# Kernel optimization log

Measured on AMD Instinct MI355X. Metric: run time of the kernel, lower is better.

## Reference

```python
import jax, jax.numpy as jnp
import numpy as np

NUM_HEADS = 12
AGENT_NUM = 49

def setup_inputs() -> dict:
    key = jax.random.key(0)
    ks = jax.random.split(key, 5)
    B, N, C = 32, 1176, 768
    x = jax.random.normal(ks[0], (B, N, C), dtype=jnp.float32)
    qkv_w = jax.random.normal(ks[1], (3 * C, C), dtype=jnp.float32) * 0.02
    qkv_b = jax.random.normal(ks[2], (3 * C,), dtype=jnp.float32) * 0.02
    proj_w = jax.random.normal(ks[3], (C, C), dtype=jnp.float32) * 0.02
    proj_b = jax.random.normal(ks[4], (C,), dtype=jnp.float32) * 0.02
    return {"x": x, "qkv_w": qkv_w, "qkv_b": qkv_b, "proj_w": proj_w,
            "proj_b": proj_b, "t_h": 14, "t_w": 14, "s_h": 28, "s_w": 28}

def _softmax_clamped(a):
    # original: float32 clamp to finfo min/max, then softmax(dim=-1)
    fi = jnp.finfo(jnp.float32)
    a = jnp.clip(a.astype(jnp.float32), fi.min, fi.max)
    return jax.nn.softmax(a, axis=-1)

def reference(x, qkv_w, qkv_b, proj_w, proj_b, t_h, t_w, s_h, s_w):
    B, N, C = x.shape
    H = NUM_HEADS
    hd = C // H
    scale = hd ** -0.5
    n_mt = 2 * t_h * t_w
    n_s = s_h * s_w

    qkv = (x @ qkv_w.T + qkv_b).reshape(B, N, 3, H, hd).transpose(2, 0, 3, 1, 4)
    q, k, v = qkv[0], qkv[1], qkv[2]  # [B,H,N,hd]

    q_mt, q_s = q[:, :, :n_mt], q[:, :, n_mt:]
    k_mt = k[:, :, :n_mt]
    v_mt = v[:, :, :n_mt]

    # stage 1: template/memory self-attention
    attn = _softmax_clamped(jnp.einsum('bhqd,bhkd->bhqk', q_mt, k_mt) * scale)
    x_mt = jnp.einsum('bhqk,bhkd->bhqd', attn, v_mt).transpose(0, 2, 1, 3).reshape(B, n_mt, C)

    # agent tokens: pool q_s (replicates original layout-scrambling reshape)
    p = int(AGENT_NUM ** 0.5)  # 7
    agent = q_s.reshape(B, s_h, s_w, C).transpose(0, 3, 1, 2)  # [B,C,s_h,s_w]
    agent = agent.reshape(B, C, p, s_h // p, p, s_w // p).mean(axis=(3, 5))  # exact AdaptiveAvgPool2d(7,7)
    agent = agent.reshape(B, C, AGENT_NUM).transpose(0, 2, 1)  # [B,agent_num,C]
    agent = agent.reshape(B, AGENT_NUM, H, hd).transpose(0, 2, 1, 3)  # [B,H,agent_num,hd]

    # stage 2: agent attends to all keys
    agent_attn = _softmax_clamped(jnp.einsum('bhad,bhkd->bhak', agent * scale, k))
    agent_v = jnp.einsum('bhak,bhkd->bhad', agent_attn, v)  # [B,H,agent_num,hd]

    # stage 3: search queries attend to agent tokens
    q_attn = _softmax_clamped(jnp.einsum('bhqd,bhad->bhqa', q_s * scale, agent))
    x_s = jnp.einsum('bhqa,bhad->bhqd', q_attn, agent_v).transpose(0, 2, 1, 3).reshape(B, n_s, C)

    out = jnp.concatenate([x_mt, x_s], axis=1)
    out = out @ proj_w.T + proj_b
    return out
```

## Files before the change

kernel.cpp:

```cpp
#include <hip/hip_runtime.h>

typedef __attribute__((ext_vector_type(8))) short short8;
typedef __attribute__((ext_vector_type(4))) short short4v;
typedef __attribute__((ext_vector_type(4))) float f32x4;
typedef unsigned short u16;

#define B_    32
#define N_    1176
#define C_    768
#define H_    12
#define HD_   64
#define NMT_  392
#define AG_   49
#define NEGBIG_ (-1.0e4f)

__device__ __forceinline__ u16 f2bf(float f) {
  unsigned u = __float_as_uint(f);
  unsigned r = (u + 0x7fffu + ((u >> 16) & 1u)) >> 16;
  return (u16)r;
}
__device__ __forceinline__ float bf2f(u16 s) {
  return __uint_as_float(((unsigned)s) << 16);
}

__device__ __forceinline__ int xcd_swz(int g, int nwg) {
  const int q = nwg >> 3, r = nwg & 7;
  const int xcd = g & 7, off = g >> 3;
  return (xcd < r ? xcd * (q + 1) : r * (q + 1) + (xcd - r) * q) + off;
}

template <int LO>
__global__ __launch_bounds__(256) void splitf(const float* __restrict__ in,
                                              u16* __restrict__ hi,
                                              u16* __restrict__ lo, int n4) {
  int i = blockIdx.x * 256 + threadIdx.x;
  const int stride = gridDim.x * 256;
  for (; i < n4; i += stride) {
    const float4 v = ((const float4*)in)[i];
    const float f[4] = {v.x, v.y, v.z, v.w};
    short4v h, l;
#pragma unroll
    for (int e = 0; e < 4; ++e) {
      u16 hb = f2bf(f[e]);
      h[e] = (short)hb;
      if (LO) l[e] = (short)f2bf(f[e] - bf2f(hb));
    }
    ((short4v*)hi)[i] = h;
    if (LO) ((short4v*)lo)[i] = l;
  }
}

__global__ __launch_bounds__(256, 3) void gemm_qkv(
    const u16* __restrict__ A, const u16* __restrict__ Bw,
    const float* __restrict__ bias, u16* __restrict__ qb, u16* __restrict__ kb,
    u16* __restrict__ vb, int Mch) {
  __shared__ u16 SH[17408];
  u16* As = SH;
  u16* Bs = SH + 8192;
  const int tid = threadIdx.x;
  const int swz = xcd_swz(blockIdx.x, gridDim.x);
  const int brow = swz / 18, bcol = swz - brow * 18;
  const int m0 = brow * 128, c0 = bcol * 128;
  const int lane = tid & 63, w = tid >> 6;
  const int wr = w >> 1, wc = w & 1;
  const int fr = lane & 15, ko = lane >> 4;
  const int lsw = (lane * 8) ^ (ko << 4);

  f32x4 acc[4][4];
#pragma unroll
  for (int m = 0; m < 4; ++m)
#pragma unroll
    for (int n = 0; n < 4; ++n) acc[m][n] = (f32x4)0.f;

  short8 ra[4], rb[4];
  auto LOADG = [&](int kt) {
#pragma unroll
    for (int i = 0; i < 4; ++i) {
      const int ch = tid + i * 256;
      const int row = ch >> 3, slotk = ch & 7;
      const int ar = min(m0 + row, Mch - 1);
      ra[i] = *(const short8*)&A[(size_t)ar * 768 + kt * 64 + slotk * 8];
      rb[i] = *(const short8*)&Bw[(size_t)(c0 + row) * 768 + kt * 64 + slotk * 8];
    }
  };
  auto WRITE = [&]() {
#pragma unroll
    for (int i = 0; i < 4; ++i) {
      const int ch = tid + i * 256;
      const int row = ch >> 3, slotk = ch & 7;
      const int s = slotk >> 2, sl = slotk & 3;
      const int off = (row >> 4) * 1024 + s * 512 +
                      ((sl * 128 + (row & 15) * 8) ^ (sl << 4));
      *(short8*)&As[off] = ra[i];
      *(short8*)&Bs[off] = rb[i];
    }
  };

  LOADG(0);
  for (int kt = 0; kt < 12; ++kt) {
    __syncthreads();
    WRITE();
    if (kt < 11) LOADG(kt + 1);
    __syncthreads();
#pragma unroll
    for (int s = 0; s < 2; ++s) {
      short8 af[4], bfr[4];
#pragma unroll
      for (int m = 0; m < 4; ++m)
        af[m] = *(const short8*)&As[((wr * 4 + m) * 2 + s) * 512 + lsw];
#pragma unroll
      for (int n = 0; n < 4; ++n)
        bfr[n] = *(const short8*)&Bs[((wc * 4 + n) * 2 + s) * 512 + lsw];
#pragma unroll
      for (int m = 0; m < 4; ++m)
#pragma unroll
        for (int n = 0; n < 4; ++n)
          acc[m][n] = __builtin_amdgcn_mfma_f32_16x16x32_bf16(af[m], bfr[n], acc[m][n], 0, 0, 0);
    }
  }

  __syncthreads();
  const int t = c0 / 768;
  const int hbase = (c0 % 768) >> 6;
  if (t < 2) {
#pragma unroll
    for (int n = 0; n < 4; ++n) {
      const int col = wc * 64 + n * 16 + fr;
      const float bv = bias[c0 + col];
#pragma unroll
      for (int m = 0; m < 4; ++m)
#pragma unroll
        for (int r = 0; r < 4; ++r) {
          const int row = wr * 64 + m * 16 + ko * 4 + r;
          SH[row * 136 + col] = f2bf(acc[m][n][r] + bv);
        }
    }
    __syncthreads();
    u16* dst = (t == 0) ? qb : kb;
    for (int it = tid; it < 2048; it += 256) {
      const int rt = it >> 4, half = (it >> 3) & 1, p = it & 7;
      const int mg = m0 + rt;
      if (mg < Mch) {
        const int bl = mg / N_, nt = mg - bl * N_;
        const short8 vv = *(const short8*)&SH[rt * 136 + half * 64 + p * 8];
        *(short8*)&dst[(((size_t)bl * H_ + hbase + half) * N_ + nt) * 64 + p * 8] = vv;
      }
    }
  } else {
#pragma unroll
    for (int n = 0; n < 4; ++n) {
      const int col = wc * 64 + n * 16 + fr;
      const float bv = bias[c0 + col];
#pragma unroll
      for (int m = 0; m < 4; ++m)
#pragma unroll
        for (int r = 0; r < 4; ++r) {
          const int row = wr * 64 + m * 16 + ko * 4 + r;
          SH[col * 136 + row] = f2bf(acc[m][n][r] + bv);
        }
    }
    __syncthreads();
    for (int it = tid; it < 2048; it += 256) {
      const int ct = it >> 4, tc = it & 15;
      const int mg0 = m0 + tc * 8;
      if (mg0 < Mch) {
        const int bl = mg0 / N_, nt = mg0 - bl * N_;
        const int d = ct & 63, hh = hbase + (ct >> 6);
        const short8 vv = *(const short8*)&SH[ct * 136 + tc * 8];
        *(short8*)&vb[(((size_t)bl * H_ + hh) * 64 + d) * N_ + nt] = vv;
      }
    }
  }
}

__global__ __launch_bounds__(256, 2) void gemm_proj(
    const u16* __restrict__ Ahg, const u16* __restrict__ Alg,
    const u16* __restrict__ Bhg, const u16* __restrict__ Blg,
    const float* __restrict__ bias, float* __restrict__ out) {
  __shared__ u16 Ah[8192], Al[8192], Bh[8192], Bl[8192];
  const int tid = threadIdx.x;
  const int swz = xcd_swz(blockIdx.x, gridDim.x);
  const int brow = swz / 6, bcol = swz - brow * 6;
  const int m0 = brow * 128, c0 = bcol * 128;
  const int lane = tid & 63, w = tid >> 6;
  const int wr = w >> 1, wc = w & 1;
  const int fr = lane & 15, ko = lane >> 4;
  const int lsw = (lane * 8) ^ (ko << 4);

  f32x4 acc[4][4];
#pragma unroll
  for (int m = 0; m < 4; ++m)
#pragma unroll
    for (int n = 0; n < 4; ++n) acc[m][n] = (f32x4)0.f;

  short8 rah[4], ral[4], rbh[4], rbl[4];
  auto LOADG = [&](int kt) {
#pragma unroll
    for (int i = 0; i < 4; ++i) {
      const int ch = tid + i * 256;
      const int row = ch >> 3, slotk = ch & 7;
      const size_t aoff = (size_t)(m0 + row) * 768 + kt * 64 + slotk * 8;
      const size_t boff = (size_t)(c0 + row) * 768 + kt * 64 + slotk * 8;
      rah[i] = *(const short8*)&Ahg[aoff];
      ral[i] = *(const short8*)&Alg[aoff];
      rbh[i] = *(const short8*)&Bhg[boff];
      rbl[i] = *(const short8*)&Blg[boff];
    }
  };
  auto WRITE = [&]() {
#pragma unroll
    for (int i = 0; i < 4; ++i) {
      const int ch = tid + i * 256;
      const int row = ch >> 3, slotk = ch & 7;
      const int s = slotk >> 2, sl = slotk & 3;
      const int off = (row >> 4) * 1024 + s * 512 +
                      ((sl * 128 + (row & 15) * 8) ^ (sl << 4));
      *(short8*)&Ah[off] = rah[i];
      *(short8*)&Al[off] = ral[i];
      *(short8*)&Bh[off] = rbh[i];
      *(short8*)&Bl[off] = rbl[i];
    }
  };

  LOADG(0);
  for (int kt = 0; kt < 12; ++kt) {
    __syncthreads();
    WRITE();
    if (kt < 11) LOADG(kt + 1);
    __syncthreads();
#pragma unroll
    for (int s = 0; s < 2; ++s) {
      short8 ah[4], al[4], bh[4], bl[4];
#pragma unroll
      for (int m = 0; m < 4; ++m) {
        const int off = ((wr * 4 + m) * 2 + s) * 512 + lsw;
        ah[m] = *(const short8*)&Ah[off];
        al[m] = *(const short8*)&Al[off];
      }
#pragma unroll
      for (int n = 0; n < 4; ++n) {
        const int off = ((wc * 4 + n) * 2 + s) * 512 + lsw;
        bh[n] = *(const short8*)&Bh[off];
        bl[n] = *(const short8*)&Bl[off];
      }
#pragma unroll
      for (int m = 0; m < 4; ++m)
#pragma unroll
        for (int n = 0; n < 4; ++n) {
          acc[m][n] = __builtin_amdgcn_mfma_f32_16x16x32_bf16(ah[m], bh[n], acc[m][n], 0, 0, 0);
          acc[m][n] = __builtin_amdgcn_mfma_f32_16x16x32_bf16(ah[m], bl[n], acc[m][n], 0, 0, 0);
          acc[m][n] = __builtin_amdgcn_mfma_f32_16x16x32_bf16(al[m], bh[n], acc[m][n], 0, 0, 0);
        }
    }
  }
#pragma unroll
  for (int n = 0; n < 4; ++n) {
    const int col = c0 + wc * 64 + n * 16 + fr;
    const float bv = bias[col];
#pragma unroll
    for (int m = 0; m < 4; ++m) {
      const int mg = m0 + wr * 64 + m * 16 + ko * 4;
#pragma unroll
      for (int r = 0; r < 4; ++r) out[(size_t)(mg + r) * 768 + col] = acc[m][n][r] + bv;
    }
  }
}

__global__ __launch_bounds__(256) void agent_pool(const u16* __restrict__ q,
                                                  u16* __restrict__ agent) {
  const int wid = threadIdx.x >> 6;
  const int lane = threadIdx.x & 63;
  const int row = blockIdx.x * 4 + wid;
  const int rem = row % (H_ * 64);
  const int b = row / (H_ * 64);
  const int h2 = rem / 64;
  const int a = rem % 64;
  if (a >= AG_) {
    agent[((size_t)b * H_ + h2) * 4096 + a * 64 + lane] = 0;
    return;
  }
  const int ap = a / 7, aq = a % 7;
  float s = 0.f;
#pragma unroll
  for (int i = 0; i < 4; ++i)
#pragma unroll
    for (int j = 0; j < 4; ++j) {
      const int g = (ap * 4 + i) * 336 + (aq * 4 + j) * 12 + h2;
      const int h = g / 784, n = g % 784;
      s += bf2f(q[(((size_t)b * H_ + h) * N_ + NMT_ + n) * HD_ + lane]);
    }
  agent[((size_t)b * H_ + h2) * 4096 + a * 64 + lane] = f2bf(s * 0.0625f);
}

__global__ __launch_bounds__(256, 3) void flash_attn(
    const u16* __restrict__ Q, int q_bh_str, int q_base, int q_row_max, int q_valid,
    const u16* __restrict__ K, int k_bh_str, int k_row_max,
    const u16* __restrict__ Vt, int vt_bh_str, int vt_pitch, int vt_col_max,
    int n_keys, int nkt,
    u16* __restrict__ cch, u16* __restrict__ ccl, int b0,
    u16* __restrict__ avT, int mode) {
  __shared__ u16 Qs[4096], Ks[4096], Vts[4096], Ps[4096];
  __shared__ float Ss[64][65];
  __shared__ float mS[64], lS[64], aS[64];

  const int tid = threadIdx.x, bh = blockIdx.x;
  const int q0 = q_base + blockIdx.y * 56;
  const int lane = tid & 63, w = tid >> 6;
  const int fr = lane & 15, ko = lane >> 4;

  const u16* Qb = Q + (size_t)bh * q_bh_str;
  const u16* Kb = K + (size_t)bh * k_bh_str;
  const u16* Vb = Vt + (size_t)bh * vt_bh_str;

#pragma unroll
  for (int i = 0; i < 2; ++i) {
    const int ch = tid + i * 256;
    const int row = ch >> 3, c8 = (ch & 7) << 3;
    const int qr = min(q0 + row, q_row_max);
    const short8 v = *(const short8*)&Qb[(size_t)qr * 64 + c8];
    *(short8*)&Qs[(row * 64 + c8) ^ ((row & 7) << 3)] = v;
  }
  if (tid < 64) { mS[tid] = NEGBIG_; lS[tid] = 0.f; aS[tid] = 0.f; }

  f32x4 oacc[4];
#pragma unroll
  for (int d = 0; d < 4; ++d) oacc[d] = (f32x4)0.f;

  for (int kt = 0; kt < nkt; ++kt) {
#pragma unroll
    for (int i = 0; i < 2; ++i) {
      const int ch = tid + i * 256;
      const int row = ch >> 3, c8 = (ch & 7) << 3;
      const int kr = min(kt * 64 + row, k_row_max);
      const short8 v = *(const short8*)&Kb[(size_t)kr * 64 + c8];
      *(short8*)&Ks[(row * 64 + c8) ^ ((row & 7) << 3)] = v;
    }
#pragma unroll
    for (int i = 0; i < 2; ++i) {
      const int ch = tid + i * 256;
      const int row = ch >> 3, c8 = (ch & 7) << 3;
      const int col8 = kt * 64 + c8;
      const u16* src = &Vb[(size_t)row * vt_pitch];
      short8 v;
      if (col8 + 8 <= vt_col_max) {
        v = *(const short8*)&src[col8];
      } else {
#pragma unroll
        for (int e = 0; e < 8; ++e) v[e] = (short)src[min(col8 + e, vt_col_max - 1)];
      }
      *(short8*)&Vts[(row * 64 + c8) ^ ((row & 7) << 3)] = v;
    }
    __syncthreads();

    short8 aq[2];
#pragma unroll
    for (int s = 0; s < 2; ++s)
      aq[s] = *(const short8*)&Qs[((w * 16 + fr) * 64 + s * 32 + ko * 8) ^ ((fr & 7) << 3)];
#pragma unroll
    for (int j = 0; j < 4; ++j) {
      f32x4 sa = (f32x4)0.f;
#pragma unroll
      for (int s = 0; s < 2; ++s) {
        const short8 bk = *(const short8*)&Ks[((j * 16 + fr) * 64 + s * 32 + ko * 8) ^ ((fr & 7) << 3)];
        sa = __builtin_amdgcn_mfma_f32_16x16x32_bf16(aq[s], bk, sa, 0, 0, 0);
      }
      const int colg = kt * 64 + j * 16 + fr;
      const bool maskc = (colg >= n_keys);
#pragma unroll
      for (int r = 0; r < 4; ++r) {
        const int srow = w * 16 + ko * 4 + r;
        Ss[srow][j * 16 + fr] = maskc ? NEGBIG_ : sa[r] * 0.125f;
      }
    }
    __syncthreads();

    {
      const int r = tid >> 2, jj = tid & 3;
      float sv[16];
      float mx = NEGBIG_;
#pragma unroll
      for (int c = 0; c < 16; ++c) {
        sv[c] = Ss[r][jj * 16 + c];
        mx = fmaxf(mx, sv[c]);
      }
      mx = fmaxf(mx, __shfl_xor(mx, 1));
      mx = fmaxf(mx, __shfl_xor(mx, 2));
      const float mold = mS[r];
      const float mnew = fmaxf(mold, mx);
      float sum = 0.f;
#pragma unroll
      for (int c = 0; c < 16; ++c) {
        const bool mk = (kt * 64 + jj * 16 + c) >= n_keys;
        const float p = mk ? 0.f : __expf(sv[c] - mnew);
        sum += p;
        Ps[(r * 64 + jj * 16 + c) ^ ((r & 7) << 3)] = f2bf(p);
      }
      sum += __shfl_xor(sum, 1);
      sum += __shfl_xor(sum, 2);
      if (jj == 0) {
        const float alpha = __expf(mold - mnew);
        aS[r] = alpha;
        lS[r] = lS[r] * alpha + sum;
        mS[r] = mnew;
      }
    }
    __syncthreads();

    float al[4];
#pragma unroll
    for (int r = 0; r < 4; ++r) al[r] = aS[w * 16 + ko * 4 + r];
    short8 ap[2];
#pragma unroll
    for (int s = 0; s < 2; ++s)
      ap[s] = *(const short8*)&Ps[((w * 16 + fr) * 64 + s * 32 + ko * 8) ^ ((fr & 7) << 3)];
#pragma unroll
    for (int dj = 0; dj < 4; ++dj) {
      f32x4 o = oacc[dj];
#pragma unroll
      for (int r = 0; r < 4; ++r) o[r] *= al[r];
#pragma unroll
      for (int s = 0; s < 2; ++s) {
        const short8 bv = *(const short8*)&Vts[((dj * 16 + fr) * 64 + s * 32 + ko * 8) ^ ((fr & 7) << 3)];
        o = __builtin_amdgcn_mfma_f32_16x16x32_bf16(ap[s], bv, o, 0, 0, 0);
      }
      oacc[dj] = o;
    }
    __syncthreads();
  }

  float linv[4];
#pragma unroll
  for (int r = 0; r < 4; ++r) linv[r] = 1.f / fmaxf(lS[w * 16 + ko * 4 + r], 1e-30f);

  if (mode == 0) {
    const int b = bh / H_, h = bh % H_;
#pragma unroll
    for (int dj = 0; dj < 4; ++dj)
#pragma unroll
      for (int r = 0; r < 4; ++r) {
        const int rowl = w * 16 + ko * 4 + r;
        if (rowl < q_valid) {
          const size_t m = (size_t)(b0 + b) * N_ + q0 + rowl;
          const float val = oacc[dj][r] * linv[r];
          const u16 hb = f2bf(val);
          const u16 lb = f2bf(val - bf2f(hb));
          const size_t idx = m * 768 + h * 64 + dj * 16 + fr;
          cch[idx] = hb;
          ccl[idx] = lb;
        }
      }
  } else {
#pragma unroll
    for (int dj = 0; dj < 4; ++dj)
#pragma unroll
      for (int r = 0; r < 4; ++r) {
        const int a = w * 16 + ko * 4 + r;
        avT[(size_t)bh * 4096 + (dj * 16 + fr) * 64 + a] = f2bf(oacc[dj][r] * linv[r]);
      }
  }
}

extern "C" void kernel_launch(void* const* d_in, const int* in_sizes, int n_in,
                              void* d_out, int out_size, void* d_ws,
                              size_t ws_size, hipStream_t stream) {
  const float* x = (const float*)d_in[0];
  const float* qkv_w = (const float*)d_in[1];
  const float* qkv_b = (const float*)d_in[2];
  const float* proj_w = (const float*)d_in[3];
  const float* proj_b = (const float*)d_in[4];
  float* out = (float*)d_out;
  u16* ws = (u16*)d_ws;

  const size_t XBF = 28901376ull;
  const size_t QW = 2304ull * 768;
  const size_t PW = 768ull * 768;
  const size_t QKV1 = (size_t)H_ * N_ * HD_;
  const size_t AG1 = (size_t)H_ * 64 * 64;

  size_t o = 0;
  u16* xbf = ws + o; o += XBF;
  u16* qwh = ws + o; o += QW;
  u16* pwh = ws + o; o += PW;
  u16* pwl = ws + o; o += PW;
  u16* cch = ws + o; o += XBF;
  u16* ccl = ws + o; o += XBF;
  const size_t fixed_sh = o;
  const size_t per_sh = 3 * QKV1 + 2 * AG1;

  int cb = 1;
  const int cands[6] = {32, 16, 8, 4, 2, 1};
  for (int i = 0; i < 6; ++i)
    if ((fixed_sh + (size_t)cands[i] * per_sh) * 2 <= ws_size) { cb = cands[i]; break; }

  u16* qb = ws + o; o += cb * QKV1;
  u16* kb = ws + o; o += cb * QKV1;
  u16* vb = ws + o; o += cb * QKV1;
  u16* agent = ws + o; o += cb * AG1;
  u16* avT = ws + o; o += cb * AG1;

  splitf<0><<<2048, 256, 0, stream>>>(x, xbf, nullptr, (int)(XBF / 4));
  splitf<0><<<1024, 256, 0, stream>>>(qkv_w, qwh, nullptr, (int)(QW / 4));
  splitf<1><<<512, 256, 0, stream>>>(proj_w, pwh, pwl, (int)(PW / 4));

  const int nch = B_ / cb;
  for (int chn = 0; chn < nch; ++chn) {
    const int b0 = chn * cb;
    const int Mch = cb * N_;
    const int nrow = (Mch + 127) / 128;
    gemm_qkv<<<dim3(nrow * 18), 256, 0, stream>>>(
        xbf + (size_t)b0 * N_ * 768, qwh, qkv_b, qb, kb, vb, Mch);
    agent_pool<<<dim3(cb * 192), 256, 0, stream>>>(qb, agent);
    flash_attn<<<dim3(cb * H_, 1), 256, 0, stream>>>(
        agent, 4096, 0, 48, AG_, kb, N_ * HD_, N_ - 1,
        vb, N_ * HD_, N_, N_, N_, 19, nullptr, nullptr, b0, avT, 1);
    flash_attn<<<dim3(cb * H_, 7), 256, 0, stream>>>(
        qb, N_ * HD_, 0, N_ - 1, 56, kb, N_ * HD_, N_ - 1,
        vb, N_ * HD_, N_, N_, NMT_, 7, cch, ccl, b0, nullptr, 0);
    flash_attn<<<dim3(cb * H_, 14), 256, 0, stream>>>(
        qb, N_ * HD_, NMT_, N_ - 1, 56, agent, 4096, 63,
        avT, 4096, 64, 64, AG_, 1, cch, ccl, b0, nullptr, 0);
  }
  gemm_proj<<<dim3(294 * 6), 256, 0, stream>>>(cch, ccl, pwh, pwl, proj_b, out);
}
```

Measured before the change: 537.0 us.

## Drop low-bf16 split of attention output and remap QKV GEMM block order

```diff
diff --git a/kernel.cpp b/kernel.cpp
--- a/kernel.cpp
+++ b/kernel.cpp
@@ -59,7 +59,11 @@
   u16* Bs = SH + 8192;
   const int tid = threadIdx.x;
   const int swz = xcd_swz(blockIdx.x, gridDim.x);
-  const int brow = swz / 18, bcol = swz - brow * 18;
+  const int half = gridDim.x >> 1;
+  const int cg = swz / half;
+  const int rem = swz - cg * half;
+  const int brow = rem / 9;
+  const int bcol = cg * 9 + (rem - brow * 9);
   const int m0 = brow * 128, c0 = bcol * 128;
   const int lane = tid & 63, w = tid >> 6;
   const int wr = w >> 1, wc = w & 1;
@@ -138,12 +142,12 @@
     __syncthreads();
     u16* dst = (t == 0) ? qb : kb;
     for (int it = tid; it < 2048; it += 256) {
-      const int rt = it >> 4, half = (it >> 3) & 1, p = it & 7;
+      const int rt = it >> 4, half2 = (it >> 3) & 1, p = it & 7;
       const int mg = m0 + rt;
       if (mg < Mch) {
         const int bl = mg / N_, nt = mg - bl * N_;
-        const short8 vv = *(const short8*)&SH[rt * 136 + half * 64 + p * 8];
-        *(short8*)&dst[(((size_t)bl * H_ + hbase + half) * N_ + nt) * 64 + p * 8] = vv;
+        const short8 vv = *(const short8*)&SH[rt * 136 + half2 * 64 + p * 8];
+        *(short8*)&dst[(((size_t)bl * H_ + hbase + half2) * N_ + nt) * 64 + p * 8] = vv;
       }
     }
   } else {
@@ -173,11 +177,11 @@
   }
 }
 
-__global__ __launch_bounds__(256, 2) void gemm_proj(
-    const u16* __restrict__ Ahg, const u16* __restrict__ Alg,
-    const u16* __restrict__ Bhg, const u16* __restrict__ Blg,
-    const float* __restrict__ bias, float* __restrict__ out) {
-  __shared__ u16 Ah[8192], Al[8192], Bh[8192], Bl[8192];
+__global__ __launch_bounds__(256, 3) void gemm_proj(
+    const u16* __restrict__ Ahg, const u16* __restrict__ Bhg,
+    const u16* __restrict__ Blg, const float* __restrict__ bias,
+    float* __restrict__ out) {
+  __shared__ u16 Ah[8192], Bh[8192], Bl[8192];
   const int tid = threadIdx.x;
   const int swz = xcd_swz(blockIdx.x, gridDim.x);
   const int brow = swz / 6, bcol = swz - brow * 6;
@@ -193,7 +197,7 @@
 #pragma unroll
     for (int n = 0; n < 4; ++n) acc[m][n] = (f32x4)0.f;
 
-  short8 rah[4], ral[4], rbh[4], rbl[4];
+  short8 rah[4], rbh[4], rbl[4];
   auto LOADG = [&](int kt) {
 #pragma unroll
     for (int i = 0; i < 4; ++i) {
@@ -202,7 +206,6 @@
       const size_t aoff = (size_t)(m0 + row) * 768 + kt * 64 + slotk * 8;
       const size_t boff = (size_t)(c0 + row) * 768 + kt * 64 + slotk * 8;
       rah[i] = *(const short8*)&Ahg[aoff];
-      ral[i] = *(const short8*)&Alg[aoff];
       rbh[i] = *(const short8*)&Bhg[boff];
       rbl[i] = *(const short8*)&Blg[boff];
     }
@@ -216,7 +219,6 @@
       const int off = (row >> 4) * 1024 + s * 512 +
                       ((sl * 128 + (row & 15) * 8) ^ (sl << 4));
       *(short8*)&Ah[off] = rah[i];
-      *(short8*)&Al[off] = ral[i];
       *(short8*)&Bh[off] = rbh[i];
       *(short8*)&Bl[off] = rbl[i];
     }
@@ -230,13 +232,10 @@
     __syncthreads();
 #pragma unroll
     for (int s = 0; s < 2; ++s) {
-      short8 ah[4], al[4], bh[4], bl[4];
-#pragma unroll
-      for (int m = 0; m < 4; ++m) {
-        const int off = ((wr * 4 + m) * 2 + s) * 512 + lsw;
-        ah[m] = *(const short8*)&Ah[off];
-        al[m] = *(const short8*)&Al[off];
-      }
+      short8 ah[4], bh[4], bl[4];
+#pragma unroll
+      for (int m = 0; m < 4; ++m)
+        ah[m] = *(const short8*)&Ah[((wr * 4 + m) * 2 + s) * 512 + lsw];
 #pragma unroll
       for (int n = 0; n < 4; ++n) {
         const int off = ((wc * 4 + n) * 2 + s) * 512 + lsw;
@@ -249,7 +248,6 @@
         for (int n = 0; n < 4; ++n) {
           acc[m][n] = __builtin_amdgcn_mfma_f32_16x16x32_bf16(ah[m], bh[n], acc[m][n], 0, 0, 0);
           acc[m][n] = __builtin_amdgcn_mfma_f32_16x16x32_bf16(ah[m], bl[n], acc[m][n], 0, 0, 0);
-          acc[m][n] = __builtin_amdgcn_mfma_f32_16x16x32_bf16(al[m], bh[n], acc[m][n], 0, 0, 0);
         }
     }
   }
@@ -297,7 +295,7 @@
     const u16* __restrict__ K, int k_bh_str, int k_row_max,
     const u16* __restrict__ Vt, int vt_bh_str, int vt_pitch, int vt_col_max,
     int n_keys, int nkt,
-    u16* __restrict__ cch, u16* __restrict__ ccl, int b0,
+    u16* __restrict__ cch, int b0,
     u16* __restrict__ avT, int mode) {
   __shared__ u16 Qs[4096], Ks[4096], Vts[4096], Ps[4096];
   __shared__ float Ss[64][65];
@@ -441,12 +439,7 @@
         const int rowl = w * 16 + ko * 4 + r;
         if (rowl < q_valid) {
           const size_t m = (size_t)(b0 + b) * N_ + q0 + rowl;
-          const float val = oacc[dj][r] * linv[r];
-          const u16 hb = f2bf(val);
-          const u16 lb = f2bf(val - bf2f(hb));
-          const size_t idx = m * 768 + h * 64 + dj * 16 + fr;
-          cch[idx] = hb;
-          ccl[idx] = lb;
+          cch[m * 768 + h * 64 + dj * 16 + fr] = f2bf(oacc[dj][r] * linv[r]);
         }
       }
   } else {
@@ -483,7 +476,6 @@
   u16* pwh = ws + o; o += PW;
   u16* pwl = ws + o; o += PW;
   u16* cch = ws + o; o += XBF;
-  u16* ccl = ws + o; o += XBF;
   const size_t fixed_sh = o;
   const size_t per_sh = 3 * QKV1 + 2 * AG1;
 
@@ -512,13 +504,13 @@
     agent_pool<<<dim3(cb * 192), 256, 0, stream>>>(qb, agent);
     flash_attn<<<dim3(cb * H_, 1), 256, 0, stream>>>(
         agent, 4096, 0, 48, AG_, kb, N_ * HD_, N_ - 1,
-        vb, N_ * HD_, N_, N_, N_, 19, nullptr, nullptr, b0, avT, 1);
+        vb, N_ * HD_, N_, N_, N_, 19, nullptr, b0, avT, 1);
     flash_attn<<<dim3(cb * H_, 7), 256, 0, stream>>>(
         qb, N_ * HD_, 0, N_ - 1, 56, kb, N_ * HD_, N_ - 1,
-        vb, N_ * HD_, N_, N_, NMT_, 7, cch, ccl, b0, nullptr, 0);
+        vb, N_ * HD_, N_, N_, NMT_, 7, cch, b0, nullptr, 0);
     flash_attn<<<dim3(cb * H_, 14), 256, 0, stream>>>(
         qb, N_ * HD_, NMT_, N_ - 1, 56, agent, 4096, 63,
-        avT, 4096, 64, 64, AG_, 1, cch, ccl, b0, nullptr, 0);
-  }
-  gemm_proj<<<dim3(294 * 6), 256, 0, stream>>>(cch, ccl, pwh, pwl, proj_b, out);
-}
+        avT, 4096, 64, 64, AG_, 1, cch, b0, nullptr, 0);
+  }
+  gemm_proj<<<dim3(294 * 6), 256, 0, stream>>>(cch, pwh, pwl, proj_b, out);
+}
```

Result: no change. 534.5 us (-0.5%).
